# Kernel optimization log

Hardware: AMD Instinct MI355X
Metric: run time of the kernel (lower is better)

## Reference

```python
import jax, jax.numpy as jnp
import numpy as np


def setup_inputs() -> dict:
    key = jax.random.key(0)
    k1, k2 = jax.random.split(key)
    B, Cin, Cout, M1, M2 = 32, 128, 128, 64, 65
    # complex tensors stored as (..., 2) = (real, imag), matching torch.view_as_complex layout
    inp = jax.random.normal(k1, (B, Cin, M1, M2, 2), dtype=jnp.float32)
    weight = jax.random.normal(k2, (Cin, Cout, M1, M2, 2), dtype=jnp.float32) * 0.02
    return {"input": inp, "weight": weight}


def reference(input, weight):
    # torch: einsum('bixy,ioxy->boxy', input_complex, view_as_complex(weight))
    # Complex batched matmul per (x, y) mode, contracting over in_channels i.
    xr, xi = input[..., 0], input[..., 1]      # [b, i, x, y]
    wr, wi = weight[..., 0], weight[..., 1]    # [i, o, x, y]
    rr = jnp.einsum('bixy,ioxy->boxy', xr, wr)
    ii = jnp.einsum('bixy,ioxy->boxy', xi, wi)
    ri = jnp.einsum('bixy,ioxy->boxy', xr, wi)
    ir = jnp.einsum('bixy,ioxy->boxy', xi, wr)
    out_r = rr - ii
    out_i = ri + ir
    return jnp.stack([out_r, out_i], axis=-1)  # [b, o, x, y, 2]
```

## Files before the change

### kernel.cpp

```cpp
#include <hip/hip_runtime.h>
#include <stdint.h>


typedef float f2 __attribute__((ext_vector_type(2)));

#define NB 32
#define CI 128
#define CO 128
#define OT 32
#define MODES 4160
#define MPB 8
#define KC 4
#define NCHUNK (CI / KC)
#define ABUF_F2 (KC * NB * MPB)
#define WBUF_F2 (KC * OT * MPB)
#define BUF_F2  (ABUF_F2 + WBUF_F2)

#define CFMA(acc, av, wv)                                                      \
  asm("v_pk_fma_f32 %0, %1, %2, %0 op_sel:[0,0,0] op_sel_hi:[0,1,1]"           \
      : "+v"(acc) : "v"(av), "v"(wv));                                         \
  asm("v_pk_fma_f32 %0, %1, %2, %0 op_sel:[1,1,0] op_sel_hi:[1,0,1] "          \
      "neg_lo:[1,0,0]"                                                         \
      : "+v"(acc) : "v"(av), "v"(wv));

#define VM_WAIT(N) asm volatile("s_waitcnt vmcnt(" #N ")" ::: "memory")

__device__ __forceinline__ void gload16(const f2* g, f2* l) {
    __builtin_amdgcn_global_load_lds(
        (const __attribute__((address_space(1))) uint32_t*)g,
        (__attribute__((address_space(3))) uint32_t*)l, 16, 0, 0);
}

template <int PH>
__device__ __forceinline__ void stage_phase(const f2* __restrict__ Ig,
                                            const f2* __restrict__ Wl,
                                            f2* dst, int t, int m0,
                                            int obase, int k0) {
    if constexpr (PH < 2) {
        const int j  = PH * 256 + t;
        const int kk = j >> 7, b = (j >> 2) & 31, mlp = j & 3;
        gload16(Ig + (size_t)(b * CI + k0 + kk) * MODES + m0 + mlp * 2,
                dst + j * 2);
    } else {
        const int j   = (PH - 2) * 256 + t;
        const int kk  = j >> 7, oph = (j >> 2) & 31, p = j & 3;
        const int sw  = (oph >> 3) & 3;
        const int o   = oph ^ (sw & 1);
        const int qg  = p ^ sw;
        gload16(Wl + (size_t)((k0 + kk) * CO + obase + o) * MODES + m0 + qg * 2,
                dst + ABUF_F2 + j * 2);
    }
}

__global__ __launch_bounds__(256, 4)
void cmul2d_kernel(const f2* __restrict__ Ig,
                   const f2* __restrict__ Wl,
                   f2* __restrict__ Og) {
    __shared__ f2 lds[2 * BUF_F2];

    const int t = threadIdx.x;

    const int bid   = blockIdx.x;
    const int jid   = (bid & 7) * 260 + (bid >> 3);
    const int mg    = jid >> 2;
    const int oq    = jid & 3;
    const int m0    = mg * MPB;
    const int obase = oq * OT;

    const int ml = t & 7;
    const int s  = t >> 3;
    const int so = s & 3;
    const int sb = s >> 2;

    f2 acc[4][8];
#pragma unroll
    for (int r = 0; r < 4; ++r)
#pragma unroll
        for (int q = 0; q < 8; ++q) acc[r][q] = (f2)(0.0f);

    const int pxor = (ml >> 1);

    stage_phase<0>(Ig, Wl, lds, t, m0, obase, 0);
    stage_phase<1>(Ig, Wl, lds, t, m0, obase, 0);
    stage_phase<2>(Ig, Wl, lds, t, m0, obase, 0);
    stage_phase<3>(Ig, Wl, lds, t, m0, obase, 0);

#pragma unroll 1
    for (int c = 0; c < NCHUNK; ++c) {
        VM_WAIT(0);
        __builtin_amdgcn_s_barrier();
        __builtin_amdgcn_sched_barrier(0);

        const f2* Ab = lds + (c & 1) * BUF_F2;
        const f2* Wb = Ab + ABUF_F2;
        f2* nbuf = lds + ((c + 1) & 1) * BUF_F2;
        const bool more = (c + 1 < NCHUNK);
        const int  nk0  = (c + 1) * KC;

#pragma unroll
        for (int kk = 0; kk < KC; ++kk) {
            f2 a[4], w[8];
#pragma unroll
            for (int r = 0; r < 4; ++r)
                a[r] = Ab[kk * (NB * MPB) + (sb * 4 + r) * MPB + ml];
#pragma unroll
            for (int q = 0; q < 8; ++q) {
                const int o   = so * 8 + q;
                const int oph = o ^ (so & 1);
                const int p   = pxor ^ so;
                w[q] = Wb[(kk * (OT * MPB)) + ((oph * 4 + p) << 1) + (ml & 1)];
            }
            if (more) {
                if (kk == 0) stage_phase<0>(Ig, Wl, nbuf, t, m0, obase, nk0);
                else if (kk == 1) stage_phase<1>(Ig, Wl, nbuf, t, m0, obase, nk0);
                else if (kk == 2) stage_phase<2>(Ig, Wl, nbuf, t, m0, obase, nk0);
                else stage_phase<3>(Ig, Wl, nbuf, t, m0, obase, nk0);
            }
            __builtin_amdgcn_s_setprio(1);
#pragma unroll
            for (int r = 0; r < 4; ++r)
#pragma unroll
                for (int q = 0; q < 8; ++q) {
                    CFMA(acc[r][q], a[r], w[q]);
                }
            __builtin_amdgcn_s_setprio(0);
        }
    }

#pragma unroll
    for (int r = 0; r < 4; ++r) {
        const int b = sb * 4 + r;
#pragma unroll
        for (int q = 0; q < 8; ++q) {
            const int o = obase + so * 8 + q;
            Og[(size_t)(b * CO + o) * MODES + m0 + ml] = acc[r][q];
        }
    }
}

extern "C" void kernel_launch(void* const* d_in, const int* in_sizes, int n_in,
                              void* d_out, int out_size, void* d_ws, size_t ws_size,
                              hipStream_t stream) {
    const f2* I = (const f2*)d_in[0];
    const f2* W = (const f2*)d_in[1];
    f2* O = (f2*)d_out;
    dim3 grid(2080);
    dim3 block(256);
    cmul2d_kernel<<<grid, block, 0, stream>>>(I, W, O);
}
```

Baseline: 253.9 us.

## Halve output-channel tile to 16 and double grid with higher occupancy

```diff
diff --git a/kernel.cpp b/kernel.cpp
--- a/kernel.cpp
+++ b/kernel.cpp
@@ -7,7 +7,7 @@
 #define NB 32
 #define CI 128
 #define CO 128
-#define OT 32
+#define OT 16
 #define MODES 4160
 #define MPB 8
 #define KC 4
@@ -31,59 +31,54 @@
         (__attribute__((address_space(3))) uint32_t*)l, 16, 0, 0);
 }
 
-template <int PH>
-__device__ __forceinline__ void stage_phase(const f2* __restrict__ Ig,
-                                            const f2* __restrict__ Wl,
-                                            f2* dst, int t, int m0,
-                                            int obase, int k0) {
-    if constexpr (PH < 2) {
-        const int j  = PH * 256 + t;
-        const int kk = j >> 7, b = (j >> 2) & 31, mlp = j & 3;
-        gload16(Ig + (size_t)(b * CI + k0 + kk) * MODES + m0 + mlp * 2,
-                dst + j * 2);
+template <int U>
+__device__ __forceinline__ void stage_unit(const f2* __restrict__ Ig,
+                                           const f2* __restrict__ Wl,
+                                           f2* dst, int t, int m0,
+                                           int obase, int k0) {
+    if constexpr (U < 2) {
+        const int u  = U * 256 + t;
+        const int kk = u >> 7, b = (u >> 2) & 31, mu = u & 3;
+        gload16(Ig + (size_t)(b * CI + k0 + kk) * MODES + m0 + mu * 2,
+                dst + u * 2);
     } else {
-        const int j   = (PH - 2) * 256 + t;
-        const int kk  = j >> 7, oph = (j >> 2) & 31, p = j & 3;
-        const int sw  = (oph >> 3) & 3;
-        const int o   = oph ^ (sw & 1);
-        const int qg  = p ^ sw;
-        gload16(Wl + (size_t)((k0 + kk) * CO + obase + o) * MODES + m0 + qg * 2,
-                dst + ABUF_F2 + j * 2);
+        const int kk = t >> 6, oph = (t >> 2) & 15, mu = t & 3;
+        const int o  = oph ^ ((oph >> 2) & 1);
+        gload16(Wl + (size_t)((k0 + kk) * CO + obase + o) * MODES + m0 + mu * 2,
+                dst + ABUF_F2 + t * 2);
     }
 }
 
-__global__ __launch_bounds__(256, 4)
+__global__ __launch_bounds__(256, 6)
 void cmul2d_kernel(const f2* __restrict__ Ig,
                    const f2* __restrict__ Wl,
                    f2* __restrict__ Og) {
     __shared__ f2 lds[2 * BUF_F2];
 
-    const int t = threadIdx.x;
+    const int t   = threadIdx.x;
+    const int bid = blockIdx.x;
 
-    const int bid   = blockIdx.x;
-    const int jid   = (bid & 7) * 260 + (bid >> 3);
-    const int mg    = jid >> 2;
-    const int oq    = jid & 3;
-    const int m0    = mg * MPB;
-    const int obase = oq * OT;
+    const int g   = bid & 7;
+    const int l   = bid >> 3;
+    const int mgl = l >> 3;
+    const int oj  = l & 7;
+    const int m0    = (g * 65 + mgl) * MPB;
+    const int obase = oj * OT;
 
     const int ml = t & 7;
     const int s  = t >> 3;
     const int so = s & 3;
     const int sb = s >> 2;
 
-    f2 acc[4][8];
+    f2 acc[4][4];
 #pragma unroll
     for (int r = 0; r < 4; ++r)
 #pragma unroll
-        for (int q = 0; q < 8; ++q) acc[r][q] = (f2)(0.0f);
+        for (int q = 0; q < 4; ++q) acc[r][q] = (f2)(0.0f);
 
-    const int pxor = (ml >> 1);
-
-    stage_phase<0>(Ig, Wl, lds, t, m0, obase, 0);
-    stage_phase<1>(Ig, Wl, lds, t, m0, obase, 0);
-    stage_phase<2>(Ig, Wl, lds, t, m0, obase, 0);
-    stage_phase<3>(Ig, Wl, lds, t, m0, obase, 0);
+    stage_unit<0>(Ig, Wl, lds, t, m0, obase, 0);
+    stage_unit<1>(Ig, Wl, lds, t, m0, obase, 0);
+    stage_unit<2>(Ig, Wl, lds, t, m0, obase, 0);
 
 #pragma unroll 1
     for (int c = 0; c < NCHUNK; ++c) {
@@ -99,28 +94,25 @@
 
 #pragma unroll
         for (int kk = 0; kk < KC; ++kk) {
-            f2 a[4], w[8];
+            f2 a[4], w[4];
 #pragma unroll
             for (int r = 0; r < 4; ++r)
                 a[r] = Ab[kk * (NB * MPB) + (sb * 4 + r) * MPB + ml];
 #pragma unroll
-            for (int q = 0; q < 8; ++q) {
-                const int o   = so * 8 + q;
-                const int oph = o ^ (so & 1);
-                const int p   = pxor ^ so;
-                w[q] = Wb[(kk * (OT * MPB)) + ((oph * 4 + p) << 1) + (ml & 1)];
+            for (int q = 0; q < 4; ++q) {
+                const int oph = (so * 4 + q) ^ (so & 1);
+                w[q] = Wb[kk * (OT * MPB) + oph * MPB + ml];
             }
             if (more) {
-                if (kk == 0) stage_phase<0>(Ig, Wl, nbuf, t, m0, obase, nk0);
-                else if (kk == 1) stage_phase<1>(Ig, Wl, nbuf, t, m0, obase, nk0);
-                else if (kk == 2) stage_phase<2>(Ig, Wl, nbuf, t, m0, obase, nk0);
-                else stage_phase<3>(Ig, Wl, nbuf, t, m0, obase, nk0);
+                if (kk == 0) stage_unit<0>(Ig, Wl, nbuf, t, m0, obase, nk0);
+                else if (kk == 1) stage_unit<1>(Ig, Wl, nbuf, t, m0, obase, nk0);
+                else if (kk == 2) stage_unit<2>(Ig, Wl, nbuf, t, m0, obase, nk0);
             }
             __builtin_amdgcn_s_setprio(1);
 #pragma unroll
             for (int r = 0; r < 4; ++r)
 #pragma unroll
-                for (int q = 0; q < 8; ++q) {
+                for (int q = 0; q < 4; ++q) {
                     CFMA(acc[r][q], a[r], w[q]);
                 }
             __builtin_amdgcn_s_setprio(0);
@@ -131,8 +123,8 @@
     for (int r = 0; r < 4; ++r) {
         const int b = sb * 4 + r;
 #pragma unroll
-        for (int q = 0; q < 8; ++q) {
-            const int o = obase + so * 8 + q;
+        for (int q = 0; q < 4; ++q) {
+            const int o = obase + so * 4 + q;
             Og[(size_t)(b * CO + o) * MODES + m0 + ml] = acc[r][q];
         }
     }
@@ -144,7 +136,7 @@
     const f2* I = (const f2*)d_in[0];
     const f2* W = (const f2*)d_in[1];
     f2* O = (f2*)d_out;
-    dim3 grid(2080);
+    dim3 grid(4160);
     dim3 block(256);
     cmul2d_kernel<<<grid, block, 0, stream>>>(I, W, O);
 }
```

Measured after the change: 262.8 us. 1.04x slower.
